# Optimization experiments

Measured on AMD Instinct MI355X. Metric: run time of the kernel, lower is better.

The kernel has to match this reference:

```python
import jax, jax.numpy as jnp
import numpy as np


def _normal_distance(n1, n2):
    # Cosine-style normal distance: 1 - <n1, n2>. The original module stubs
    # this as 0; we use the canonical mesh-normal loss so the cdist+argmin+
    # gather chain is exercised end-to-end.
    return 1.0 - jnp.sum(n1 * n2, axis=-1)


def setup_inputs() -> dict:
    key = jax.random.key(0)
    k1, k2, k3, k4 = jax.random.split(key, 4)
    N, M = 8192, 32768
    pred_pts = jax.random.normal(k1, (1, N, 3), dtype=jnp.float32)
    pred_nrm = jax.random.normal(k2, (1, N, 3), dtype=jnp.float32)
    gt_pts = jax.random.normal(k3, (1, M, 3), dtype=jnp.float32)
    gt_nrm = jax.random.normal(k4, (1, M, 3), dtype=jnp.float32)
    # unit normals, as on a real mesh
    pred_nrm = pred_nrm / jnp.linalg.norm(pred_nrm, axis=-1, keepdims=True)
    gt_nrm = gt_nrm / jnp.linalg.norm(gt_nrm, axis=-1, keepdims=True)
    return {
        "predicted_points_batch": pred_pts,
        "predicted_normals_batch": pred_nrm,
        "gt_points_batch": gt_pts,
        "gt_normals_batch": gt_nrm,
    }


def reference(predicted_points_batch, predicted_normals_batch,
              gt_points_batch, gt_normals_batch):
    # Original forward returns inside the first loop iteration -> element 0 only.
    p = predicted_points_batch[0]    # [N,3]
    pn = predicted_normals_batch[0]  # [N,3]
    g = gt_points_batch[0]           # [M,3]
    gn = gt_normals_batch[0]         # [M,3]

    # Squared pairwise distances (monotone in true cdist; only argmin is used).
    # d2[i,j] = |p_i|^2 + |g_j|^2 - 2 p_i . g_j   -> one [N,M] intermediate.
    d2 = (jnp.sum(p * p, axis=1)[:, None]
          + jnp.sum(g * g, axis=1)[None, :]
          - 2.0 * (p @ g.T))                      # [N,M]

    gt_idx = jnp.argmin(d2, axis=1)    # nearest gt point per predicted point, [N]
    pr_idx = jnp.argmin(d2, axis=0)    # nearest predicted point per gt point, [M]

    nearest_gt_normals = gn[gt_idx]    # [N,3]
    nearest_pr_normals = pn[pr_idx]    # [M,3]

    dist1 = _normal_distance(pn, nearest_gt_normals)  # [N]
    dist2 = _normal_distance(gn, nearest_pr_normals)  # [M]
    return jnp.mean(dist1) + jnp.mean(dist2)
```

## Files before the change

kernel.cpp:

```cpp
#include <hip/hip_runtime.h>
#include <stdint.h>

#define BLK 256
#define IPT 8
#define OWNERS (BLK * IPT)
#define SLICE 256

typedef unsigned long long ull;

__device__ __forceinline__ unsigned int ford(float f) {
    int b = __float_as_int(f);
    return (b >= 0) ? ((unsigned)b ^ 0x80000000u) : ~(unsigned)b;
}

__global__ __launch_bounds__(BLK) void nn_argmin_dual(
    const float* __restrict__ p, const float* __restrict__ g,
    ull* __restrict__ rowmin, ull* __restrict__ colmin,
    int rowBlocks, int rowSlices, int colSlices)
{
    __shared__ float4 sb[SLICE];

    const float* A; const float* B; ull* outmin; int id, nSlices;
    if ((int)blockIdx.x < rowBlocks) {
        id = blockIdx.x;             A = p; B = g; outmin = rowmin; nSlices = rowSlices;
    } else {
        id = blockIdx.x - rowBlocks; A = g; B = p; outmin = colmin; nSlices = colSlices;
    }
    const int chunk = id / nSlices;
    const int slice = id - chunk * nSlices;
    const int s0 = slice * SLICE;

    if (threadIdx.x < SLICE) {
        int s = s0 + threadIdx.x;
        float bx = B[3 * s], by = B[3 * s + 1], bz = B[3 * s + 2];
        sb[threadIdx.x] = make_float4(bx, by, bz, bx * bx + by * by + bz * bz);
    }

    const int o0 = chunk * OWNERS + threadIdx.x;
    float ax[IPT], ay[IPT], az[IPT], best[IPT];
    int bidx[IPT];
#pragma unroll
    for (int r = 0; r < IPT; ++r) {
        int o = o0 + r * BLK;
        ax[r] = -2.0f * A[3 * o];
        ay[r] = -2.0f * A[3 * o + 1];
        az[r] = -2.0f * A[3 * o + 2];
        best[r] = __int_as_float(0x7f7fffff);
        bidx[r] = 0;
    }
    __syncthreads();

#pragma unroll 4
    for (int k = 0; k < SLICE; ++k) {
        float4 q = sb[k];
        int sj = s0 + k;
#pragma unroll
        for (int r = 0; r < IPT; ++r) {
            float v = fmaf(ax[r], q.x, fmaf(ay[r], q.y, fmaf(az[r], q.z, q.w)));
            if (v < best[r]) { best[r] = v; bidx[r] = sj; }
        }
    }

#pragma unroll
    for (int r = 0; r < IPT; ++r) {
        ull packed = ((ull)ford(best[r]) << 32) | (unsigned)bidx[r];
        atomicMin(&outmin[o0 + r * BLK], packed);
    }
}

__global__ __launch_bounds__(BLK) void finalize_kernel(
    const ull* __restrict__ rowmin, const ull* __restrict__ colmin,
    const float* __restrict__ pn, const float* __restrict__ gn,
    float* __restrict__ out, int N, int M, float invN, float invM)
{
    int t = blockIdx.x * BLK + threadIdx.x;
    float c = 0.0f;
    if (t < N) {
        int j = (int)(rowmin[t] & 0xffffffffull);
        float d = pn[3 * t] * gn[3 * j] + pn[3 * t + 1] * gn[3 * j + 1]
                + pn[3 * t + 2] * gn[3 * j + 2];
        c = (1.0f - d) * invN;
    } else if (t < N + M) {
        int j = t - N;
        int i = (int)(colmin[j] & 0xffffffffull);
        float d = gn[3 * j] * pn[3 * i] + gn[3 * j + 1] * pn[3 * i + 1]
                + gn[3 * j + 2] * pn[3 * i + 2];
        c = (1.0f - d) * invM;
    }
#pragma unroll
    for (int off = 32; off > 0; off >>= 1) c += __shfl_down(c, off, 64);
    __shared__ float partial[BLK / 64];
    if ((threadIdx.x & 63) == 0) partial[threadIdx.x >> 6] = c;
    __syncthreads();
    if (threadIdx.x == 0) {
        float s = 0.0f;
#pragma unroll
        for (int w = 0; w < BLK / 64; ++w) s += partial[w];
        atomicAdd(out, s);
    }
}

extern "C" void kernel_launch(void* const* d_in, const int* in_sizes, int n_in,
                              void* d_out, int out_size, void* d_ws, size_t ws_size,
                              hipStream_t stream) {
    const float* p  = (const float*)d_in[0];
    const float* pn = (const float*)d_in[1];
    const float* g  = (const float*)d_in[2];
    const float* gn = (const float*)d_in[3];
    const int N = in_sizes[0] / 3;
    const int M = in_sizes[2] / 3;

    ull* rowmin = (ull*)d_ws;
    ull* colmin = rowmin + N;
    float* out = (float*)d_out;

    hipMemsetAsync(d_ws, 0xFF, (size_t)(N + M) * sizeof(ull), stream);
    hipMemsetAsync(d_out, 0, sizeof(float), stream);

    const int rowSlices = M / SLICE;
    const int colSlices = N / SLICE;
    const int rowBlocks = (N / OWNERS) * rowSlices;
    const int colBlocks = (M / OWNERS) * colSlices;
    nn_argmin_dual<<<rowBlocks + colBlocks, BLK, 0, stream>>>(
        p, g, rowmin, colmin, rowBlocks, rowSlices, colSlices);

    int tot = N + M;
    finalize_kernel<<<(tot + BLK - 1) / BLK, BLK, 0, stream>>>(
        rowmin, colmin, pn, gn, out, N, M, 1.0f / N, 1.0f / M);
}
```

Before: 124.7 us.

## Track only min value in hot loop, recover argmin index in finalize pass

The inner distance loop now keeps only a running min with fminf, and records just the 64-wide sub-block where the min improved instead of tracking a per-candidate index. The finalize kernel recomputes the 64 distances in that sub-block to find the exact index whose value equals the stored min. This removes the compare-and-select index bookkeeping from the hot loop. The slice size is halved, which doubles the number of blocks and atomics. Tie-breaking may differ from first-index argmin, and the float-equality rematch relies on bitwise-identical recomputation.

```diff
diff --git a/kernel.cpp b/kernel.cpp
--- a/kernel.cpp
+++ b/kernel.cpp
@@ -1,10 +1,12 @@
 #include <hip/hip_runtime.h>
 #include <stdint.h>
+#include <float.h>
 
 #define BLK 256
 #define IPT 8
 #define OWNERS (BLK * IPT)
-#define SLICE 256
+#define SLICE 128
+#define SUB 64
 
 typedef unsigned long long ull;
 
@@ -12,8 +14,12 @@
     int b = __float_as_int(f);
     return (b >= 0) ? ((unsigned)b ^ 0x80000000u) : ~(unsigned)b;
 }
+__device__ __forceinline__ float ford_inv(unsigned int u) {
+    int b = (u & 0x80000000u) ? (int)(u ^ 0x80000000u) : (int)~u;
+    return __int_as_float(b);
+}
 
-__global__ __launch_bounds__(BLK) void nn_argmin_dual(
+__global__ __launch_bounds__(BLK) void nn_min_dual(
     const float* __restrict__ p, const float* __restrict__ g,
     ull* __restrict__ rowmin, ull* __restrict__ colmin,
     int rowBlocks, int rowSlices, int colSlices)
@@ -33,59 +39,81 @@
     if (threadIdx.x < SLICE) {
         int s = s0 + threadIdx.x;
         float bx = B[3 * s], by = B[3 * s + 1], bz = B[3 * s + 2];
-        sb[threadIdx.x] = make_float4(bx, by, bz, bx * bx + by * by + bz * bz);
+        float w = fmaf(bz, bz, fmaf(by, by, bx * bx));
+        sb[threadIdx.x] = make_float4(bx, by, bz, w);
     }
 
     const int o0 = chunk * OWNERS + threadIdx.x;
     float ax[IPT], ay[IPT], az[IPT], best[IPT];
-    int bidx[IPT];
+    int base[IPT];
 #pragma unroll
     for (int r = 0; r < IPT; ++r) {
         int o = o0 + r * BLK;
         ax[r] = -2.0f * A[3 * o];
         ay[r] = -2.0f * A[3 * o + 1];
         az[r] = -2.0f * A[3 * o + 2];
-        best[r] = __int_as_float(0x7f7fffff);
-        bidx[r] = 0;
+        best[r] = FLT_MAX;
+        base[r] = s0;
     }
     __syncthreads();
 
+    for (int st = 0; st < SLICE; st += SUB) {
+        float prev[IPT];
+#pragma unroll
+        for (int r = 0; r < IPT; ++r) prev[r] = best[r];
 #pragma unroll 4
-    for (int k = 0; k < SLICE; ++k) {
-        float4 q = sb[k];
-        int sj = s0 + k;
+        for (int k = st; k < st + SUB; ++k) {
+            float4 q = sb[k];
 #pragma unroll
-        for (int r = 0; r < IPT; ++r) {
-            float v = fmaf(ax[r], q.x, fmaf(ay[r], q.y, fmaf(az[r], q.z, q.w)));
-            if (v < best[r]) { best[r] = v; bidx[r] = sj; }
+            for (int r = 0; r < IPT; ++r) {
+                float v = fmaf(ax[r], q.x, fmaf(ay[r], q.y, fmaf(az[r], q.z, q.w)));
+                best[r] = fminf(best[r], v);
+            }
         }
+#pragma unroll
+        for (int r = 0; r < IPT; ++r)
+            if (best[r] < prev[r]) base[r] = s0 + st;
     }
 
 #pragma unroll
     for (int r = 0; r < IPT; ++r) {
-        ull packed = ((ull)ford(best[r]) << 32) | (unsigned)bidx[r];
+        ull packed = ((ull)ford(best[r]) << 32) | (unsigned)base[r];
         atomicMin(&outmin[o0 + r * BLK], packed);
     }
 }
 
 __global__ __launch_bounds__(BLK) void finalize_kernel(
     const ull* __restrict__ rowmin, const ull* __restrict__ colmin,
+    const float* __restrict__ p, const float* __restrict__ g,
     const float* __restrict__ pn, const float* __restrict__ gn,
     float* __restrict__ out, int N, int M, float invN, float invM)
 {
     int t = blockIdx.x * BLK + threadIdx.x;
     float c = 0.0f;
-    if (t < N) {
-        int j = (int)(rowmin[t] & 0xffffffffull);
-        float d = pn[3 * t] * gn[3 * j] + pn[3 * t + 1] * gn[3 * j + 1]
-                + pn[3 * t + 2] * gn[3 * j + 2];
-        c = (1.0f - d) * invN;
-    } else if (t < N + M) {
-        int j = t - N;
-        int i = (int)(colmin[j] & 0xffffffffull);
-        float d = gn[3 * j] * pn[3 * i] + gn[3 * j + 1] * pn[3 * i + 1]
-                + gn[3 * j + 2] * pn[3 * i + 2];
-        c = (1.0f - d) * invM;
+    if (t < N + M) {
+        const float* A; const float* B; const float* An; const float* Bn;
+        ull packed; int o; float inv;
+        if (t < N) { o = t;     A = p; B = g; An = pn; Bn = gn; packed = rowmin[o]; inv = invN; }
+        else       { o = t - N; A = g; B = p; An = gn; Bn = pn; packed = colmin[o]; inv = invM; }
+
+        float ax = -2.0f * A[3 * o];
+        float ay = -2.0f * A[3 * o + 1];
+        float az = -2.0f * A[3 * o + 2];
+        float bestf = ford_inv((unsigned int)(packed >> 32));
+        int base = (int)(packed & 0xffffffffull);
+
+        int idx = base;
+        for (int j = 0; j < SUB; ++j) {
+            int s = base + j;
+            float bx = B[3 * s], by = B[3 * s + 1], bz = B[3 * s + 2];
+            float w = fmaf(bz, bz, fmaf(by, by, bx * bx));
+            float v = fmaf(ax, bx, fmaf(ay, by, fmaf(az, bz, w)));
+            if (v == bestf) { idx = s; break; }
+        }
+
+        float d = An[3 * o] * Bn[3 * idx] + An[3 * o + 1] * Bn[3 * idx + 1]
+                + An[3 * o + 2] * Bn[3 * idx + 2];
+        c = (1.0f - d) * inv;
     }
 #pragma unroll
     for (int off = 32; off > 0; off >>= 1) c += __shfl_down(c, off, 64);
@@ -121,10 +149,10 @@
     const int colSlices = N / SLICE;
     const int rowBlocks = (N / OWNERS) * rowSlices;
     const int colBlocks = (M / OWNERS) * colSlices;
-    nn_argmin_dual<<<rowBlocks + colBlocks, BLK, 0, stream>>>(
+    nn_min_dual<<<rowBlocks + colBlocks, BLK, 0, stream>>>(
         p, g, rowmin, colmin, rowBlocks, rowSlices, colSlices);
 
     int tot = N + M;
     finalize_kernel<<<(tot + BLK - 1) / BLK, BLK, 0, stream>>>(
-        rowmin, colmin, pn, gn, out, N, M, 1.0f / N, 1.0f / M);
+        rowmin, colmin, p, g, pn, gn, out, N, M, 1.0f / N, 1.0f / M);
 }
```

After: 114.9 us. -7.8%, faster.
